# Kernel tuning notes

Measured on AMD Instinct MI355X. Metric: run time of the kernel, lower is better.

The kernel has to match this reference:

```python
import jax, jax.numpy as jnp
import numpy as np

N, B, D = 8, 4096, 1024
LOG_2PI = np.float32(np.log(2.0 * np.pi))


def setup_inputs() -> dict:
    key = jax.random.key(0)
    k1, k2 = jax.random.split(key)
    means = jax.random.normal(k1, (N, B, D), dtype=jnp.float32)
    logsigmas = jax.random.normal(k2, (N, B, D), dtype=jnp.float32)
    return {"means": means, "logsigmas": logsigmas}


def reference(means, logsigmas):
    # Sequential product of diagonal Gaussians.
    # Original builds DxD diag matrices + MVN log_prob; mathematically this is
    # purely elementwise over D plus a sum for the log-normalizer.
    m0, lv0 = means[0], logsigmas[0]
    lz0 = jnp.zeros(means.shape[1], dtype=means.dtype)

    def step(carry, inp):
        m1, lv1, lz = carry          # prior mean, log-variance, accumulated log_z
        m2, lv2 = inp                # next component
        v1 = jnp.exp(lv1)
        v2 = jnp.exp(lv2)
        iv1 = 1.0 / v1
        iv2 = 1.0 / v2
        cvar = 1.0 / (iv1 + iv2)              # combined variance (diag of C)
        cmean = cvar * (m1 * iv1 + m2 * iv2)  # combined mean
        s = v1 + v2 + 1e-6                    # covariance of the normalizer Gaussian
        # MVN(m2, diag(s)).log_prob(m1) == sum of univariate normal log-pdfs
        log_z = -0.5 * jnp.sum((m1 - m2) ** 2 / s + jnp.log(s) + LOG_2PI, axis=-1)
        return (cmean, jnp.log(cvar), lz + log_z), None

    (post_mean, post_logvar, log_z_total), _ = jax.lax.scan(
        step, (m0, lv0, lz0), (means[1:], logsigmas[1:])
    )
    return post_mean, post_logvar, log_z_total
```

## Files before the change

kernel.cpp:

```cpp
#include <hip/hip_runtime.h>
#include <math.h>

#define NN 8
#define BB 4096
#define DD 1024
#define LOG_2PI 1.8378770664093453f


typedef float f32x4 __attribute__((ext_vector_type(4)));

__global__ __launch_bounds__(256) void mpc_kernel(
    const float* __restrict__ means,
    const float* __restrict__ logsig,
    float* __restrict__ out_mean,
    float* __restrict__ out_logvar,
    float* __restrict__ out_logz)
{
    const int t    = threadIdx.x;
    const int wave = t >> 6;
    const int lane = t & 63;
    const int row  = (blockIdx.x << 2) + wave;
    const size_t plane   = (size_t)BB * DD;
    const size_t rowbase = (size_t)row * DD;
    const int off = lane * 4;

    f32x4 bm[2][4], bl[2][4];

#pragma unroll
    for (int k = 0; k < 4; ++k) {
        bm[0][k] = *(const f32x4*)(means  + rowbase + k * 256 + off);
        bl[0][k] = *(const f32x4*)(logsig + rowbase + k * 256 + off);
    }

    float m1[16], v1[16], iv1[16];
    float z = 0.0f;

#pragma unroll
    for (int n = 0; n < NN; ++n) {
        if (n + 1 < NN) {
            const size_t pb = (size_t)(n + 1) * plane + rowbase;
#pragma unroll
            for (int k = 0; k < 4; ++k) {
                bm[(n + 1) & 1][k] = *(const f32x4*)(means  + pb + k * 256 + off);
                bl[(n + 1) & 1][k] = *(const f32x4*)(logsig + pb + k * 256 + off);
            }
        }
        __builtin_amdgcn_sched_barrier(0);

#pragma unroll
        for (int k = 0; k < 4; ++k) {
            const float mk[4] = {bm[n & 1][k].x, bm[n & 1][k].y,
                                 bm[n & 1][k].z, bm[n & 1][k].w};
            const float lk[4] = {bl[n & 1][k].x, bl[n & 1][k].y,
                                 bl[n & 1][k].z, bl[n & 1][k].w};
#pragma unroll
            for (int j = 0; j < 4; ++j) {
                const int e = k * 4 + j;
                if (n == 0) {
                    m1[e]  = mk[j];
                    v1[e]  = __expf(lk[j]);
                    iv1[e] = __expf(-lk[j]);
                } else {
                    float v2   = __expf(lk[j]);
                    float iv2  = __expf(-lk[j]);
                    float s    = v1[e] + v2 + 1e-6f;
                    float d    = m1[e] - mk[j];
                    z += d * d * __builtin_amdgcn_rcpf(s) + __logf(s);
                    float ivn  = iv1[e] + iv2;
                    float cv   = __builtin_amdgcn_rcpf(ivn);
                    m1[e]  = cv * (m1[e] * iv1[e] + mk[j] * iv2);
                    v1[e]  = cv;
                    iv1[e] = ivn;
                }
            }
        }
    }

#pragma unroll
    for (int k = 0; k < 4; ++k) {
        f32x4 om = {m1[k*4+0], m1[k*4+1], m1[k*4+2], m1[k*4+3]};
        f32x4 ol = {__logf(v1[k*4+0]), __logf(v1[k*4+1]),
                    __logf(v1[k*4+2]), __logf(v1[k*4+3])};
        __builtin_nontemporal_store(om, (f32x4*)(out_mean   + rowbase + k * 256 + off));
        __builtin_nontemporal_store(ol, (f32x4*)(out_logvar + rowbase + k * 256 + off));
    }

#pragma unroll
    for (int o = 32; o > 0; o >>= 1)
        z += __shfl_down(z, o, 64);
    if (lane == 0)
        out_logz[row] = -0.5f * (z + (float)((NN - 1) * DD) * LOG_2PI);
}

extern "C" void kernel_launch(void* const* d_in, const int* in_sizes, int n_in,
                              void* d_out, int out_size, void* d_ws, size_t ws_size,
                              hipStream_t stream) {
    const float* means  = (const float*)d_in[0];
    const float* logsig = (const float*)d_in[1];
    float* out = (float*)d_out;
    float* out_mean   = out;
    float* out_logvar = out + (size_t)BB * DD;
    float* out_logz   = out + 2 * (size_t)BB * DD;
    mpc_kernel<<<BB / 4, 256, 0, stream>>>(means, logsig, out_mean, out_logvar, out_logz);
}
```

Before: 291.8 us.

## Split each row across two waves to halve registers and raise occupancy

Each wave now processes half of a row (512 elements) instead of a full row, so per-thread register arrays shrink and the grid doubles. A launch-bounds occupancy hint is added. The two half-row partial log-normalizer sums are combined through shared memory with a block barrier. The aim is more waves in flight to hide global load latency in this bandwidth-bound kernel, at the cost of a small shared-memory reduction and a sync.

After: 376.7 us. +29.1%, slower.

```diff
diff --git a/kernel.cpp b/kernel.cpp
--- a/kernel.cpp
+++ b/kernel.cpp
@@ -9,7 +9,7 @@
 
 typedef float f32x4 __attribute__((ext_vector_type(4)));
 
-__global__ __launch_bounds__(256) void mpc_kernel(
+__global__ __launch_bounds__(256, 5) void mpc_kernel(
     const float* __restrict__ means,
     const float* __restrict__ logsig,
     float* __restrict__ out_mean,
@@ -19,36 +19,35 @@
     const int t    = threadIdx.x;
     const int wave = t >> 6;
     const int lane = t & 63;
-    const int row  = (blockIdx.x << 2) + wave;
-    const size_t plane   = (size_t)BB * DD;
-    const size_t rowbase = (size_t)row * DD;
-    const int off = lane * 4;
+    const int h    = (blockIdx.x << 2) + wave;
+    const int row  = h >> 1;
+    const size_t plane = (size_t)BB * DD;
+    const size_t base = (size_t)row * DD + (size_t)(h & 1) * 512 + (size_t)lane * 4;
 
-    f32x4 bm[2][4], bl[2][4];
-
+    f32x4 bm[2][2], bl[2][2];
 #pragma unroll
-    for (int k = 0; k < 4; ++k) {
-        bm[0][k] = *(const f32x4*)(means  + rowbase + k * 256 + off);
-        bl[0][k] = *(const f32x4*)(logsig + rowbase + k * 256 + off);
+    for (int k = 0; k < 2; ++k) {
+        bm[0][k] = *(const f32x4*)(means  + base + k * 256);
+        bl[0][k] = *(const f32x4*)(logsig + base + k * 256);
     }
 
-    float m1[16], v1[16], iv1[16];
+    float m1[8], v1[8], iv1[8];
     float z = 0.0f;
 
 #pragma unroll
     for (int n = 0; n < NN; ++n) {
         if (n + 1 < NN) {
-            const size_t pb = (size_t)(n + 1) * plane + rowbase;
+            const size_t pb = (size_t)(n + 1) * plane + base;
 #pragma unroll
-            for (int k = 0; k < 4; ++k) {
-                bm[(n + 1) & 1][k] = *(const f32x4*)(means  + pb + k * 256 + off);
-                bl[(n + 1) & 1][k] = *(const f32x4*)(logsig + pb + k * 256 + off);
+            for (int k = 0; k < 2; ++k) {
+                bm[(n + 1) & 1][k] = *(const f32x4*)(means  + pb + k * 256);
+                bl[(n + 1) & 1][k] = *(const f32x4*)(logsig + pb + k * 256);
             }
         }
         __builtin_amdgcn_sched_barrier(0);
 
 #pragma unroll
-        for (int k = 0; k < 4; ++k) {
+        for (int k = 0; k < 2; ++k) {
             const float mk[4] = {bm[n & 1][k].x, bm[n & 1][k].y,
                                  bm[n & 1][k].z, bm[n & 1][k].w};
             const float lk[4] = {bl[n & 1][k].x, bl[n & 1][k].y,
@@ -77,19 +76,25 @@
     }
 
 #pragma unroll
-    for (int k = 0; k < 4; ++k) {
+    for (int k = 0; k < 2; ++k) {
         f32x4 om = {m1[k*4+0], m1[k*4+1], m1[k*4+2], m1[k*4+3]};
         f32x4 ol = {__logf(v1[k*4+0]), __logf(v1[k*4+1]),
                     __logf(v1[k*4+2]), __logf(v1[k*4+3])};
-        __builtin_nontemporal_store(om, (f32x4*)(out_mean   + rowbase + k * 256 + off));
-        __builtin_nontemporal_store(ol, (f32x4*)(out_logvar + rowbase + k * 256 + off));
+        __builtin_nontemporal_store(om, (f32x4*)(out_mean   + base + k * 256));
+        __builtin_nontemporal_store(ol, (f32x4*)(out_logvar + base + k * 256));
     }
 
 #pragma unroll
     for (int o = 32; o > 0; o >>= 1)
         z += __shfl_down(z, o, 64);
-    if (lane == 0)
-        out_logz[row] = -0.5f * (z + (float)((NN - 1) * DD) * LOG_2PI);
+
+    __shared__ float sz[4];
+    if (lane == 0) sz[wave] = z;
+    __syncthreads();
+    if (lane == 0 && (wave & 1) == 0) {
+        float total = sz[wave] + sz[wave + 1];
+        out_logz[row] = -0.5f * (total + (float)((NN - 1) * DD) * LOG_2PI);
+    }
 }
 
 extern "C" void kernel_launch(void* const* d_in, const int* in_sizes, int n_in,
@@ -101,5 +106,5 @@
     float* out_mean   = out;
     float* out_logvar = out + (size_t)BB * DD;
     float* out_logz   = out + 2 * (size_t)BB * DD;
-    mpc_kernel<<<BB / 4, 256, 0, stream>>>(means, logsig, out_mean, out_logvar, out_logz);
+    mpc_kernel<<<BB * 2 / 4, 256, 0, stream>>>(means, logsig, out_mean, out_logvar, out_logz);
 }
```
